# Kernel tuning notes

Measured on AMD Instinct MI355X. Metric: run time of the kernel, lower is better.

## Reference

```python
import jax, jax.numpy as jnp
import numpy as np

B, T, C, H = 256, 256, 384, 64  # batch, seq (== block_size), n_embd, head_size


def setup_inputs() -> dict:
    key = jax.random.key(0)
    kx, kk, kq, kv = jax.random.split(key, 4)
    scale = C ** -0.5
    x = jax.random.normal(kx, (B, T, C), dtype=jnp.float32)
    Wk = jax.random.normal(kk, (C, H), dtype=jnp.float32) * scale
    Wq = jax.random.normal(kq, (C, H), dtype=jnp.float32) * scale
    Wv = jax.random.normal(kv, (C, H), dtype=jnp.float32) * scale
    return {"x": x, "Wk": Wk, "Wq": Wq, "Wv": Wv}


def reference(x, Wk, Wq, Wv):
    # Single causal self-attention head (x_kv=None path). Dropout is eval-mode (identity).
    Tn = x.shape[1]
    k = x @ Wk            # [B, T, H]
    q = x @ Wq            # [B, T, H]
    v = x @ Wv            # [B, T, H]
    inv_sqrt_d = k.shape[-1] ** -0.5
    wei = jnp.einsum('bth,bsh->bts', q, k) * inv_sqrt_d  # [B, T, T]
    causal = jnp.tril(jnp.ones((Tn, Tn), dtype=bool))
    wei = jnp.where(causal, wei, -jnp.inf)
    wei = jax.nn.softmax(wei, axis=-1)
    out = jnp.einsum('bts,bsh->bth', wei, v)             # [B, T, H]
    return out
```

## Files before the change

kernel.cpp:

```cpp
#include <hip/hip_runtime.h>

#define BATCH 256
#define SEQ   256
#define CDIM  384
#define HDIM  64

typedef __attribute__((ext_vector_type(8))) short bf16x8;
typedef __attribute__((ext_vector_type(4))) float f32x4;

__device__ __forceinline__ unsigned f2bf(float f) {
  union { float f; unsigned u; } v; v.f = f;
  unsigned r = v.u + 0x7FFFu + ((v.u >> 16) & 1u);
  return r >> 16;
}

__global__ void wtrans_kernel(const float* __restrict__ Wk, const float* __restrict__ Wq,
                              const float* __restrict__ Wv, unsigned short* __restrict__ WTf) {
  int gid = blockIdx.x * 256 + threadIdx.x;
  if (gid >= 192 * CDIM) return;
  int n = gid / CDIM, kk = gid - n * CDIM;
  const float* W = (n < 64) ? Wq : (n < 128) ? Wk : Wv;
  int nt = n >> 4, ln = n & 15, ks = kk >> 5, sub = (kk >> 3) & 3, j = kk & 7;
  int lane = ln + 16 * sub;
  WTf[(((size_t)ks * 12 + nt) * 64 + lane) * 8 + j] =
      (unsigned short)f2bf(W[kk * HDIM + (n & 63)]);
}

__global__ __launch_bounds__(512, 2) void proj_kernel(
    const float* __restrict__ x, const unsigned short* __restrict__ WTf,
    unsigned short* __restrict__ qws, unsigned short* __restrict__ kws,
    unsigned short* __restrict__ vT) {
  __shared__ unsigned short wtlds[73728];
  __shared__ unsigned short vtile[64][72];
  const int tid = threadIdx.x, bid = blockIdx.x;
  const int w = tid >> 6, lane = tid & 63;
  const int ln15 = lane & 15, quad = lane >> 4;

  {
    const uint4* src = (const uint4*)WTf;
    uint4* dst = (uint4*)wtlds;
    #pragma unroll
    for (int i = 0; i < 18; ++i) dst[i * 512 + tid] = src[i * 512 + tid];
  }

  const int t0 = bid * 128 + w * 16;
  const float* xrow = x + (size_t)(t0 + ln15) * CDIM + quad * 8;
  bf16x8 bx[12];
  #pragma unroll
  for (int hh = 0; hh < 2; ++hh) {
    float4 A[12];
    #pragma unroll
    for (int j = 0; j < 6; ++j) {
      A[2 * j]     = *(const float4*)(xrow + (hh * 6 + j) * 32);
      A[2 * j + 1] = *(const float4*)(xrow + (hh * 6 + j) * 32 + 4);
    }
    #pragma unroll
    for (int j = 0; j < 6; ++j) {
      bf16x8 t;
      t[0] = (short)f2bf(A[2 * j].x);     t[1] = (short)f2bf(A[2 * j].y);
      t[2] = (short)f2bf(A[2 * j].z);     t[3] = (short)f2bf(A[2 * j].w);
      t[4] = (short)f2bf(A[2 * j + 1].x); t[5] = (short)f2bf(A[2 * j + 1].y);
      t[6] = (short)f2bf(A[2 * j + 1].z); t[7] = (short)f2bf(A[2 * j + 1].w);
      bx[hh * 6 + j] = t;
    }
  }

  __syncthreads();

  f32x4 acc[12];
  #pragma unroll
  for (int nt = 0; nt < 12; ++nt) acc[nt] = (f32x4){0.f, 0.f, 0.f, 0.f};

  #pragma unroll
  for (int ks = 0; ks < 12; ++ks) {
    #pragma unroll
    for (int nt = 0; nt < 12; ++nt) {
      bf16x8 aw = *(const bf16x8*)&wtlds[((ks * 12 + nt) * 64 + lane) * 8];
      acc[nt] = __builtin_amdgcn_mfma_f32_16x16x32_bf16(aw, bx[ks], acc[nt], 0, 0, 0);
    }
  }

  #pragma unroll
  for (int nt = 0; nt < 8; ++nt) {
    unsigned p0 = f2bf(acc[nt][0]) | (f2bf(acc[nt][1]) << 16);
    unsigned p1 = f2bf(acc[nt][2]) | (f2bf(acc[nt][3]) << 16);
    int hl = (nt & 3) * 16 + quad * 4;
    unsigned short* dst = (nt < 4) ? qws : kws;
    *(uint2*)&dst[(size_t)(t0 + ln15) * HDIM + hl] = (uint2){p0, p1};
  }

  #pragma unroll
  for (int p = 0; p < 2; ++p) {
    if ((w >> 2) == p) {
      int tl = (w & 3) * 16 + ln15;
      #pragma unroll
      for (int nt = 8; nt < 12; ++nt) {
        int hl = (nt & 3) * 16 + quad * 4;
        #pragma unroll
        for (int i = 0; i < 4; ++i)
          vtile[hl + i][tl] = (unsigned short)f2bf(acc[nt][i]);
      }
    }
    __syncthreads();
    {
      int h = tid >> 3, c = tid & 7;
      uint4 d = *(const uint4*)&vtile[h][c * 8];
      *(uint4*)&vT[((size_t)(bid >> 1) * 64 + h) * SEQ + (bid & 1) * 128 + p * 64 + c * 8] = d;
    }
    __syncthreads();
  }
}

__global__ __launch_bounds__(512, 4) void attn_kernel(
    const unsigned short* __restrict__ qws, const unsigned short* __restrict__ kws,
    const unsigned short* __restrict__ vT, float* __restrict__ out) {
  __shared__ unsigned short kl[256][72];
  __shared__ unsigned short vt[64][264];
  __shared__ unsigned short pl[8][16][36];
  const int tid = threadIdx.x;
  const int b = blockIdx.x >> 1, hgrp = blockIdx.x & 1;
  const int w = tid >> 6, lane = tid & 63;
  const int ln15 = lane & 15, quad = lane >> 4;

  for (int c = tid; c < 2048; c += 512) {
    int t = c >> 3, hc = c & 7;
    *(uint4*)&kl[t][hc * 8] = *(const uint4*)&kws[(size_t)(b * 256 + t) * HDIM + hc * 8];
  }
  for (int c = tid; c < 2048; c += 512) {
    int hh = c >> 5, tc = c & 31;
    *(uint4*)&vt[hh][tc * 8] = *(const uint4*)&vT[(size_t)(b * 64 + hh) * SEQ + tc * 8];
  }
  __syncthreads();

  const int mt = 4 * (w >> 1) + (hgrp ? (1 + (w & 1)) : (3 * (w & 1)));
  const int t0 = mt * 16;
  const int NT = (mt | 1) + 1;

  bf16x8 aq[2];
  #pragma unroll
  for (int ks = 0; ks < 2; ++ks)
    aq[ks] = *(const bf16x8*)&qws[(size_t)(b * 256 + t0 + ln15) * HDIM + ks * 32 + quad * 8];

  float sv[16][4];
  #pragma unroll
  for (int nt = 0; nt < 16; ++nt) {
    if (nt < NT) {
      f32x4 acc = (f32x4){0.f, 0.f, 0.f, 0.f};
      #pragma unroll
      for (int ks = 0; ks < 2; ++ks) {
        bf16x8 bf = *(const bf16x8*)&kl[nt * 16 + ln15][ks * 32 + quad * 8];
        acc = __builtin_amdgcn_mfma_f32_16x16x32_bf16(aq[ks], bf, acc, 0, 0, 0);
      }
      int colg = nt * 16 + ln15;
      #pragma unroll
      for (int i = 0; i < 4; ++i) {
        int rowg = t0 + quad * 4 + i;
        sv[nt][i] = (colg <= rowg) ? acc[i] * 0.125f : -3.0e38f;
      }
    }
  }
  float mx[4] = {-3.0e38f, -3.0e38f, -3.0e38f, -3.0e38f};
  #pragma unroll
  for (int nt = 0; nt < 16; ++nt)
    if (nt < NT) {
      #pragma unroll
      for (int i = 0; i < 4; ++i) mx[i] = fmaxf(mx[i], sv[nt][i]);
    }
  #pragma unroll
  for (int i = 0; i < 4; ++i) {
    mx[i] = fmaxf(mx[i], __shfl_xor(mx[i], 8, 64));
    mx[i] = fmaxf(mx[i], __shfl_xor(mx[i], 4, 64));
    mx[i] = fmaxf(mx[i], __shfl_xor(mx[i], 2, 64));
    mx[i] = fmaxf(mx[i], __shfl_xor(mx[i], 1, 64));
  }
  float sm[4] = {0.f, 0.f, 0.f, 0.f};
  #pragma unroll
  for (int nt = 0; nt < 16; ++nt)
    if (nt < NT) {
      #pragma unroll
      for (int i = 0; i < 4; ++i) {
        float e = __expf(sv[nt][i] - mx[i]);
        sv[nt][i] = e;
        sm[i] += e;
      }
    }
  #pragma unroll
  for (int i = 0; i < 4; ++i) {
    sm[i] += __shfl_xor(sm[i], 8, 64);
    sm[i] += __shfl_xor(sm[i], 4, 64);
    sm[i] += __shfl_xor(sm[i], 2, 64);
    sm[i] += __shfl_xor(sm[i], 1, 64);
  }
  float inv[4];
  #pragma unroll
  for (int i = 0; i < 4; ++i) inv[i] = 1.0f / sm[i];

  f32x4 o[4];
  #pragma unroll
  for (int ont = 0; ont < 4; ++ont) o[ont] = (f32x4){0.f, 0.f, 0.f, 0.f};

  for (int kc = 0; kc < 8; ++kc) {
    if (kc * 2 < NT) {
      #pragma unroll
      for (int half = 0; half < 2; ++half) {
        int nt = kc * 2 + half;
        #pragma unroll
        for (int i = 0; i < 4; ++i)
          pl[w][quad * 4 + i][half * 16 + ln15] =
              (unsigned short)f2bf(sv[nt][i] * inv[i]);
      }
      bf16x8 pa = *(const bf16x8*)&pl[w][ln15][quad * 8];
      #pragma unroll
      for (int ont = 0; ont < 4; ++ont) {
        bf16x8 vb = *(const bf16x8*)&vt[ont * 16 + ln15][kc * 32 + quad * 8];
        o[ont] = __builtin_amdgcn_mfma_f32_16x16x32_bf16(pa, vb, o[ont], 0, 0, 0);
      }
    }
  }

  #pragma unroll
  for (int ont = 0; ont < 4; ++ont) {
    int h = ont * 16 + ln15;
    #pragma unroll
    for (int i = 0; i < 4; ++i)
      out[(size_t)(b * 256 + t0 + quad * 4 + i) * HDIM + h] = o[ont][i];
  }
}

extern "C" void kernel_launch(void* const* d_in, const int* in_sizes, int n_in,
                              void* d_out, int out_size, void* d_ws, size_t ws_size,
                              hipStream_t stream) {
  const float* x  = (const float*)d_in[0];
  const float* Wk = (const float*)d_in[1];
  const float* Wq = (const float*)d_in[2];
  const float* Wv = (const float*)d_in[3];
  float* out = (float*)d_out;

  char* ws = (char*)d_ws;
  unsigned short* WTf = (unsigned short*)ws;
  unsigned short* qws = (unsigned short*)(ws + 262144);
  unsigned short* kws = qws + (size_t)BATCH * SEQ * HDIM;
  unsigned short* vT  = kws + (size_t)BATCH * SEQ * HDIM;

  wtrans_kernel<<<(192 * CDIM + 255) / 256, 256, 0, stream>>>(Wk, Wq, Wv, WTf);
  proj_kernel<<<512, 512, 0, stream>>>(x, WTf, qws, kws, vT);
  attn_kernel<<<2 * BATCH, 512, 0, stream>>>(qws, kws, vT, out);
}
```

Before: 182.6 us.

## Double per-wave rows in projection and use online softmax in attention

The projection kernel now processes 256 rows per block (two 16-row M tiles per wave), so each weight fragment read from LDS feeds two MFMAs and the 144KB weight staging is amortized over twice the rows. The grid drops to 256 blocks with launch bounds of one block. The attention kernel switches from a full score buffer to a flash-style online softmax over 32-key chunks, cutting register pressure from the sv[16][4] array at the cost of rescaling multiplies and extra exps and shuffles per chunk. The halved projection grid may underfill the GPU's compute units.

```diff
diff --git a/kernel.cpp b/kernel.cpp
--- a/kernel.cpp
+++ b/kernel.cpp
@@ -26,7 +26,7 @@
       (unsigned short)f2bf(W[kk * HDIM + (n & 63)]);
 }
 
-__global__ __launch_bounds__(512, 2) void proj_kernel(
+__global__ __launch_bounds__(512, 1) void proj_kernel(
     const float* __restrict__ x, const unsigned short* __restrict__ WTf,
     unsigned short* __restrict__ qws, unsigned short* __restrict__ kws,
     unsigned short* __restrict__ vT) {
@@ -43,71 +43,84 @@
     for (int i = 0; i < 18; ++i) dst[i * 512 + tid] = src[i * 512 + tid];
   }
 
-  const int t0 = bid * 128 + w * 16;
-  const float* xrow = x + (size_t)(t0 + ln15) * CDIM + quad * 8;
-  bf16x8 bx[12];
-  #pragma unroll
-  for (int hh = 0; hh < 2; ++hh) {
-    float4 A[12];
-    #pragma unroll
-    for (int j = 0; j < 6; ++j) {
-      A[2 * j]     = *(const float4*)(xrow + (hh * 6 + j) * 32);
-      A[2 * j + 1] = *(const float4*)(xrow + (hh * 6 + j) * 32 + 4);
-    }
-    #pragma unroll
-    for (int j = 0; j < 6; ++j) {
-      bf16x8 t;
-      t[0] = (short)f2bf(A[2 * j].x);     t[1] = (short)f2bf(A[2 * j].y);
-      t[2] = (short)f2bf(A[2 * j].z);     t[3] = (short)f2bf(A[2 * j].w);
-      t[4] = (short)f2bf(A[2 * j + 1].x); t[5] = (short)f2bf(A[2 * j + 1].y);
-      t[6] = (short)f2bf(A[2 * j + 1].z); t[7] = (short)f2bf(A[2 * j + 1].w);
-      bx[hh * 6 + j] = t;
-    }
+  const int trow = bid * 256 + w * 32;
+  bf16x8 bx[2][12];
+  #pragma unroll
+  for (int kb = 0; kb < 2; ++kb) {
+    float4 A[2][12];
+    #pragma unroll
+    for (int m = 0; m < 2; ++m) {
+      const float* xr = x + (size_t)(trow + m * 16 + ln15) * CDIM + quad * 8;
+      #pragma unroll
+      for (int j = 0; j < 6; ++j) {
+        A[m][2 * j]     = *(const float4*)(xr + (kb * 6 + j) * 32);
+        A[m][2 * j + 1] = *(const float4*)(xr + (kb * 6 + j) * 32 + 4);
+      }
+    }
+    #pragma unroll
+    for (int m = 0; m < 2; ++m)
+      #pragma unroll
+      for (int j = 0; j < 6; ++j) {
+        bf16x8 t;
+        t[0] = (short)f2bf(A[m][2 * j].x);     t[1] = (short)f2bf(A[m][2 * j].y);
+        t[2] = (short)f2bf(A[m][2 * j].z);     t[3] = (short)f2bf(A[m][2 * j].w);
+        t[4] = (short)f2bf(A[m][2 * j + 1].x); t[5] = (short)f2bf(A[m][2 * j + 1].y);
+        t[6] = (short)f2bf(A[m][2 * j + 1].z); t[7] = (short)f2bf(A[m][2 * j + 1].w);
+        bx[m][kb * 6 + j] = t;
+      }
   }
 
   __syncthreads();
 
-  f32x4 acc[12];
-  #pragma unroll
-  for (int nt = 0; nt < 12; ++nt) acc[nt] = (f32x4){0.f, 0.f, 0.f, 0.f};
+  f32x4 acc[2][12];
+  #pragma unroll
+  for (int m = 0; m < 2; ++m)
+    #pragma unroll
+    for (int nt = 0; nt < 12; ++nt) acc[m][nt] = (f32x4){0.f, 0.f, 0.f, 0.f};
 
   #pragma unroll
   for (int ks = 0; ks < 12; ++ks) {
     #pragma unroll
     for (int nt = 0; nt < 12; ++nt) {
       bf16x8 aw = *(const bf16x8*)&wtlds[((ks * 12 + nt) * 64 + lane) * 8];
-      acc[nt] = __builtin_amdgcn_mfma_f32_16x16x32_bf16(aw, bx[ks], acc[nt], 0, 0, 0);
-    }
-  }
-
-  #pragma unroll
-  for (int nt = 0; nt < 8; ++nt) {
-    unsigned p0 = f2bf(acc[nt][0]) | (f2bf(acc[nt][1]) << 16);
-    unsigned p1 = f2bf(acc[nt][2]) | (f2bf(acc[nt][3]) << 16);
-    int hl = (nt & 3) * 16 + quad * 4;
-    unsigned short* dst = (nt < 4) ? qws : kws;
-    *(uint2*)&dst[(size_t)(t0 + ln15) * HDIM + hl] = (uint2){p0, p1};
-  }
-
-  #pragma unroll
-  for (int p = 0; p < 2; ++p) {
-    if ((w >> 2) == p) {
-      int tl = (w & 3) * 16 + ln15;
-      #pragma unroll
-      for (int nt = 8; nt < 12; ++nt) {
-        int hl = (nt & 3) * 16 + quad * 4;
+      acc[0][nt] = __builtin_amdgcn_mfma_f32_16x16x32_bf16(aw, bx[0][ks], acc[0][nt], 0, 0, 0);
+      acc[1][nt] = __builtin_amdgcn_mfma_f32_16x16x32_bf16(aw, bx[1][ks], acc[1][nt], 0, 0, 0);
+    }
+  }
+
+  #pragma unroll
+  for (int m = 0; m < 2; ++m)
+    #pragma unroll
+    for (int nt = 0; nt < 8; ++nt) {
+      unsigned p0 = f2bf(acc[m][nt][0]) | (f2bf(acc[m][nt][1]) << 16);
+      unsigned p1 = f2bf(acc[m][nt][2]) | (f2bf(acc[m][nt][3]) << 16);
+      int hl = (nt & 3) * 16 + quad * 4;
+      unsigned short* dst = (nt < 4) ? qws : kws;
+      *(uint2*)&dst[(size_t)(trow + m * 16 + ln15) * HDIM + hl] = (uint2){p0, p1};
+    }
+
+  #pragma unroll
+  for (int p = 0; p < 4; ++p) {
+    if ((w >> 1) == p) {
+      #pragma unroll
+      for (int m = 0; m < 2; ++m) {
+        int tl = (w & 1) * 32 + m * 16 + ln15;
         #pragma unroll
-        for (int i = 0; i < 4; ++i)
-          vtile[hl + i][tl] = (unsigned short)f2bf(acc[nt][i]);
+        for (int nt = 8; nt < 12; ++nt) {
+          int hl = (nt & 3) * 16 + quad * 4;
+          #pragma unroll
+          for (int i = 0; i < 4; ++i)
+            vtile[hl + i][tl] = (unsigned short)f2bf(acc[m][nt][i]);
+        }
       }
     }
     __syncthreads();
     {
       int h = tid >> 3, c = tid & 7;
       uint4 d = *(const uint4*)&vtile[h][c * 8];
-      *(uint4*)&vT[((size_t)(bid >> 1) * 64 + h) * SEQ + (bid & 1) * 128 + p * 64 + c * 8] = d;
-    }
-    __syncthreads();
+      *(uint4*)&vT[((size_t)bid * 64 + h) * SEQ + p * 64 + c * 8] = d;
+    }
+    if (p < 3) __syncthreads();
   }
 }
 
@@ -134,96 +147,86 @@
 
   const int mt = 4 * (w >> 1) + (hgrp ? (1 + (w & 1)) : (3 * (w & 1)));
   const int t0 = mt * 16;
-  const int NT = (mt | 1) + 1;
+  const int KC = ((mt | 1) + 1) >> 1;
 
   bf16x8 aq[2];
   #pragma unroll
   for (int ks = 0; ks < 2; ++ks)
     aq[ks] = *(const bf16x8*)&qws[(size_t)(b * 256 + t0 + ln15) * HDIM + ks * 32 + quad * 8];
 
-  float sv[16][4];
-  #pragma unroll
-  for (int nt = 0; nt < 16; ++nt) {
-    if (nt < NT) {
-      f32x4 acc = (f32x4){0.f, 0.f, 0.f, 0.f};
-      #pragma unroll
-      for (int ks = 0; ks < 2; ++ks) {
-        bf16x8 bf = *(const bf16x8*)&kl[nt * 16 + ln15][ks * 32 + quad * 8];
-        acc = __builtin_amdgcn_mfma_f32_16x16x32_bf16(aq[ks], bf, acc, 0, 0, 0);
-      }
-      int colg = nt * 16 + ln15;
-      #pragma unroll
-      for (int i = 0; i < 4; ++i) {
-        int rowg = t0 + quad * 4 + i;
-        sv[nt][i] = (colg <= rowg) ? acc[i] * 0.125f : -3.0e38f;
-      }
-    }
-  }
-  float mx[4] = {-3.0e38f, -3.0e38f, -3.0e38f, -3.0e38f};
-  #pragma unroll
-  for (int nt = 0; nt < 16; ++nt)
-    if (nt < NT) {
-      #pragma unroll
-      for (int i = 0; i < 4; ++i) mx[i] = fmaxf(mx[i], sv[nt][i]);
-    }
-  #pragma unroll
-  for (int i = 0; i < 4; ++i) {
-    mx[i] = fmaxf(mx[i], __shfl_xor(mx[i], 8, 64));
-    mx[i] = fmaxf(mx[i], __shfl_xor(mx[i], 4, 64));
-    mx[i] = fmaxf(mx[i], __shfl_xor(mx[i], 2, 64));
-    mx[i] = fmaxf(mx[i], __shfl_xor(mx[i], 1, 64));
-  }
-  float sm[4] = {0.f, 0.f, 0.f, 0.f};
-  #pragma unroll
-  for (int nt = 0; nt < 16; ++nt)
-    if (nt < NT) {
-      #pragma unroll
-      for (int i = 0; i < 4; ++i) {
-        float e = __expf(sv[nt][i] - mx[i]);
-        sv[nt][i] = e;
-        sm[i] += e;
-      }
-    }
-  #pragma unroll
-  for (int i = 0; i < 4; ++i) {
-    sm[i] += __shfl_xor(sm[i], 8, 64);
-    sm[i] += __shfl_xor(sm[i], 4, 64);
-    sm[i] += __shfl_xor(sm[i], 2, 64);
-    sm[i] += __shfl_xor(sm[i], 1, 64);
-  }
-  float inv[4];
-  #pragma unroll
-  for (int i = 0; i < 4; ++i) inv[i] = 1.0f / sm[i];
-
+  float m_run[4] = {-3.0e38f, -3.0e38f, -3.0e38f, -3.0e38f};
+  float l_run[4] = {0.f, 0.f, 0.f, 0.f};
   f32x4 o[4];
   #pragma unroll
   for (int ont = 0; ont < 4; ++ont) o[ont] = (f32x4){0.f, 0.f, 0.f, 0.f};
 
-  for (int kc = 0; kc < 8; ++kc) {
-    if (kc * 2 < NT) {
-      #pragma unroll
-      for (int half = 0; half < 2; ++half) {
-        int nt = kc * 2 + half;
-        #pragma unroll
-        for (int i = 0; i < 4; ++i)
-          pl[w][quad * 4 + i][half * 16 + ln15] =
-              (unsigned short)f2bf(sv[nt][i] * inv[i]);
-      }
-      bf16x8 pa = *(const bf16x8*)&pl[w][ln15][quad * 8];
-      #pragma unroll
-      for (int ont = 0; ont < 4; ++ont) {
-        bf16x8 vb = *(const bf16x8*)&vt[ont * 16 + ln15][kc * 32 + quad * 8];
-        o[ont] = __builtin_amdgcn_mfma_f32_16x16x32_bf16(pa, vb, o[ont], 0, 0, 0);
-      }
-    }
-  }
-
+  for (int kc = 0; kc < KC; ++kc) {
+    f32x4 s0 = (f32x4){0.f, 0.f, 0.f, 0.f};
+    f32x4 s1 = (f32x4){0.f, 0.f, 0.f, 0.f};
+    #pragma unroll
+    for (int ks = 0; ks < 2; ++ks) {
+      bf16x8 b0 = *(const bf16x8*)&kl[(2 * kc) * 16 + ln15][ks * 32 + quad * 8];
+      bf16x8 b1 = *(const bf16x8*)&kl[(2 * kc + 1) * 16 + ln15][ks * 32 + quad * 8];
+      s0 = __builtin_amdgcn_mfma_f32_16x16x32_bf16(aq[ks], b0, s0, 0, 0, 0);
+      s1 = __builtin_amdgcn_mfma_f32_16x16x32_bf16(aq[ks], b1, s1, 0, 0, 0);
+    }
+    int c0 = 2 * kc * 16 + ln15;
+    float pm[4];
+    #pragma unroll
+    for (int i = 0; i < 4; ++i) {
+      int rowg = t0 + quad * 4 + i;
+      float v0 = (c0 <= rowg)      ? s0[i] * 0.125f : -3.0e38f;
+      float v1 = (c0 + 16 <= rowg) ? s1[i] * 0.125f : -3.0e38f;
+      s0[i] = v0; s1[i] = v1;
+      pm[i] = fmaxf(v0, v1);
+    }
+    #pragma unroll
+    for (int i = 0; i < 4; ++i) {
+      pm[i] = fmaxf(pm[i], __shfl_xor(pm[i], 8, 64));
+      pm[i] = fmaxf(pm[i], __shfl_xor(pm[i], 4, 64));
+      pm[i] = fmaxf(pm[i], __shfl_xor(pm[i], 2, 64));
+      pm[i] = fmaxf(pm[i], __shfl_xor(pm[i], 1, 64));
+    }
+    float alpha[4], rs[4];
+    #pragma unroll
+    for (int i = 0; i < 4; ++i) {
+      float nm = fmaxf(m_run[i], pm[i]);
+      alpha[i] = __expf(m_run[i] - nm);
+      m_run[i] = nm;
+      float e0 = __expf(s0[i] - nm);
+      float e1 = __expf(s1[i] - nm);
+      rs[i] = e0 + e1;
+      pl[w][quad * 4 + i][ln15]      = (unsigned short)f2bf(e0);
+      pl[w][quad * 4 + i][16 + ln15] = (unsigned short)f2bf(e1);
+    }
+    #pragma unroll
+    for (int i = 0; i < 4; ++i) {
+      rs[i] += __shfl_xor(rs[i], 8, 64);
+      rs[i] += __shfl_xor(rs[i], 4, 64);
+      rs[i] += __shfl_xor(rs[i], 2, 64);
+      rs[i] += __shfl_xor(rs[i], 1, 64);
+      l_run[i] = l_run[i] * alpha[i] + rs[i];
+    }
+    bf16x8 pa = *(const bf16x8*)&pl[w][ln15][quad * 8];
+    #pragma unroll
+    for (int ont = 0; ont < 4; ++ont) {
+      f32x4 cacc;
+      #pragma unroll
+      for (int i = 0; i < 4; ++i) cacc[i] = o[ont][i] * alpha[i];
+      bf16x8 vb = *(const bf16x8*)&vt[ont * 16 + ln15][kc * 32 + quad * 8];
+      o[ont] = __builtin_amdgcn_mfma_f32_16x16x32_bf16(pa, vb, cacc, 0, 0, 0);
+    }
+  }
+
+  float linv[4];
+  #pragma unroll
+  for (int i = 0; i < 4; ++i) linv[i] = 1.0f / l_run[i];
   #pragma unroll
   for (int ont = 0; ont < 4; ++ont) {
     int h = ont * 16 + ln15;
     #pragma unroll
     for (int i = 0; i < 4; ++i)
-      out[(size_t)(b * 256 + t0 + quad * 4 + i) * HDIM + h] = o[ont][i];
+      out[(size_t)(b * 256 + t0 + quad * 4 + i) * HDIM + h] = o[ont][i] * linv[i];
   }
 }
 
@@ -243,6 +246,6 @@
   unsigned short* vT  = kws + (size_t)BATCH * SEQ * HDIM;
 
   wtrans_kernel<<<(192 * CDIM + 255) / 256, 256, 0, stream>>>(Wk, Wq, Wv, WTf);
-  proj_kernel<<<512, 512, 0, stream>>>(x, WTf, qws, kws, vT);
+  proj_kernel<<<BATCH, 512, 0, stream>>>(x, WTf, qws, kws, vT);
   attn_kernel<<<2 * BATCH, 512, 0, stream>>>(qws, kws, vT, out);
 }
```

New measurement: 197.9 us. 8.4% more time.
